# Performance work log

Measured on AMD Instinct MI355X. Metric: run time of the kernel, lower is better.

The kernel has to match this reference:

```python
import jax, jax.numpy as jnp
import numpy as np

D_MODEL = 1024
N_HEADS = 16
D_K = D_MODEL // N_HEADS


def setup_inputs() -> dict:
    key = jax.random.key(0)
    ks = jax.random.split(key, 12)
    B, S, D, H = 2, 2048, D_MODEL, N_HEADS
    s = 1.0 / np.sqrt(D)
    inp = {
        "x": jax.random.normal(ks[0], (B, S, D), jnp.float32),
        "Wq": jax.random.normal(ks[1], (D, D), jnp.float32) * s,
        "bq": jnp.zeros((D,), jnp.float32),
        "Wk": jax.random.normal(ks[2], (D, D), jnp.float32) * s,
        "bk": jnp.zeros((D,), jnp.float32),
        "Wv": jax.random.normal(ks[3], (D, D), jnp.float32) * s,
        "bv": jnp.zeros((D,), jnp.float32),
        "Wo": jax.random.normal(ks[4], (D, D), jnp.float32) * s,
        "bo": jnp.zeros((D,), jnp.float32),
        "Wp": jax.random.normal(ks[5], (D, H), jnp.float32) * s,
        "bp": jnp.zeros((H,), jnp.float32),
        "alpha": jax.random.normal(ks[6], (H,), jnp.float32) * 0.1,
    }
    return inp


def reference(x, Wq, bq, Wk, bk, Wv, bv, Wo, bo, Wp, bp, alpha):
    B, S, D = x.shape
    H, dk = N_HEADS, D_K
    scale = dk ** -0.5
    # projections -> (B, H, S, dk)
    Q = (x @ Wq + bq).reshape(B, S, H, dk).transpose(0, 2, 1, 3)
    K = (x @ Wk + bk).reshape(B, S, H, dk).transpose(0, 2, 1, 3)
    V = (x @ Wv + bv).reshape(B, S, H, dk).transpose(0, 2, 1, 3)
    scores = jnp.einsum("bhid,bhjd->bhij", Q, K) * scale  # (B,H,S,S)
    # phase derived from x: (B,S,H) -> (B,H,S)
    phase = (x @ Wp + bp).transpose(0, 2, 1)
    # coherence(i,j) = cos(phi_i - phi_j), per batch/head
    coherence = jnp.cos(phase[:, :, :, None] - phase[:, :, None, :])
    scores = scores + alpha[None, :, None, None] * coherence
    attn = jax.nn.softmax(scores, axis=-1)
    out = jnp.einsum("bhij,bhjd->bhid", attn, V)  # (B,H,S,dk)
    out = out.transpose(0, 2, 1, 3).reshape(B, S, D)
    return out @ Wo + bo
```

## Files before the change

kernel.cpp:

```cpp
#include <hip/hip_runtime.h>
#include <math.h>


#define S_LEN 2048
#define NHEADS 16

typedef __attribute__((ext_vector_type(8))) short short8;
typedef __attribute__((ext_vector_type(4))) float floatx4;
typedef __attribute__((ext_vector_type(2))) float float2v;
typedef __attribute__((ext_vector_type(4))) unsigned int uintx4;

__device__ inline unsigned short f2bf(float f) {
    union { float f; unsigned int i; } v; v.f = f;
    unsigned int u = v.i;
    return (unsigned short)((u + 0x7fffu + ((u >> 16) & 1u)) >> 16);
}
__device__ inline unsigned int pack2_bf16(float hi, float lo) {
    union { float f; unsigned int u; } a, b; a.f = hi; b.f = lo;
    return __builtin_amdgcn_perm(a.u, b.u, 0x07060302u);
}
__device__ inline void async_copy16(const unsigned short* src, unsigned short* dst_lds) {
    __builtin_amdgcn_global_load_lds(
        (const __attribute__((address_space(1))) unsigned int*)(src),
        (__attribute__((address_space(3))) unsigned int*)(dst_lds), 16, 0, 0);
}
__device__ inline void async_copy4(const float* src, float* dst_lds) {
    __builtin_amdgcn_global_load_lds(
        (const __attribute__((address_space(1))) unsigned int*)(src),
        (__attribute__((address_space(3))) unsigned int*)(dst_lds), 4, 0, 0);
}

__global__ __launch_bounds__(256) void prep_kernel(
    const float* __restrict__ x, const float* __restrict__ Wp,
    const float* __restrict__ bp,
    const float* __restrict__ w0, const float* __restrict__ w1,
    const float* __restrict__ w2, const float* __restrict__ w3,
    unsigned short* __restrict__ d0, unsigned short* __restrict__ d1,
    unsigned short* __restrict__ d2, unsigned short* __restrict__ d3,
    float* __restrict__ cosP, float* __restrict__ sinP,
    unsigned short* __restrict__ xb) {
    __shared__ __align__(16) unsigned short shmem[64 * 72];
    int t = threadIdx.x;
    if (blockIdx.x < 4096) {
        float* red = reinterpret_cast<float*>(shmem);
        int bid = blockIdx.x;
        int b = bid >> 11, s = bid & 2047;
        int h = t & 15, c = t >> 4;
        const float* xr = x + (size_t)bid * 1024;
        {
            float4 xv = *reinterpret_cast<const float4*>(&xr[t * 4]);
            uint2 o;
            o.x = (unsigned int)f2bf(xv.x) | ((unsigned int)f2bf(xv.y) << 16);
            o.y = (unsigned int)f2bf(xv.z) | ((unsigned int)f2bf(xv.w) << 16);
            *reinterpret_cast<uint2*>(&xb[(size_t)bid * 1024 + t * 4]) = o;
        }
        float acc = 0.f;
#pragma unroll 8
        for (int kk = 0; kk < 64; kk++) {
            int k = c * 64 + kk;
            acc += xr[k] * Wp[k * 16 + h];
        }
        red[t] = acc;
        __syncthreads();
        if (t < 16) {
            float sum = 0.f;
#pragma unroll
            for (int c2 = 0; c2 < 16; c2++) sum += red[c2 * 16 + t];
            sum += bp[t];
            float sv, cv;
            __sincosf(sum, &sv, &cv);
            size_t o = ((size_t)b * NHEADS + t) * S_LEN + s;
            cosP[o] = cv; sinP[o] = sv;
        }
    } else {
        unsigned short (*tile)[72] = reinterpret_cast<unsigned short (*)[72]>(shmem);
        int bid = blockIdx.x - 4096;
        int mat = bid >> 8;
        int tl  = bid & 255;
        int tr = tl >> 4, tc = tl & 15;
        const float* src    = (mat == 0) ? w0 : (mat == 1) ? w1 : (mat == 2) ? w2 : w3;
        unsigned short* dst = (mat == 0) ? d0 : (mat == 1) ? d1 : (mat == 2) ? d2 : d3;
        int col = t & 63, rbase = (t >> 6) * 16;
#pragma unroll
        for (int i = 0; i < 16; i++) {
            int row = rbase + i;
            tile[row][col] = f2bf(src[(size_t)(tr * 64 + row) * 1024 + tc * 64 + col]);
        }
        __syncthreads();
#pragma unroll
        for (int i = 0; i < 16; i++) {
            int row = rbase + i;
            dst[(size_t)(tc * 64 + row) * 1024 + tr * 64 + col] = tile[col][row];
        }
    }
}

template <int MT>
__global__ __launch_bounds__(256) void gemm_bt(
    const unsigned short* __restrict__ A, const unsigned short* __restrict__ BT,
    int N, int mode,
    const float* __restrict__ b0, const float* __restrict__ b1,
    const float* __restrict__ b2,
    unsigned short* __restrict__ o0, unsigned short* __restrict__ o1,
    unsigned short* __restrict__ o2, float* __restrict__ of) {
    __shared__ __align__(16) unsigned short As[MT * 32];
    __shared__ __align__(16) unsigned short Bs[128 * 32];
    const int K = 1024;
    const int MI = MT / 32;
    int t = threadIdx.x;
    int mBase = blockIdx.x * MT;
    int nBase = blockIdx.y * 128;
    int w = t >> 6, lane = t & 63, l15 = lane & 15, quad = lane >> 4;
    int wm = (w & 1) * (MT / 2), wn = (w >> 1) * 64;
    floatx4 acc[MI][4];
#pragma unroll
    for (int i = 0; i < MI; i++)
#pragma unroll
        for (int j = 0; j < 4; j++) acc[i][j] = (floatx4){0.f, 0.f, 0.f, 0.f};

    int arow = t >> 2, aseg = (t & 3) * 8;
    for (int k0 = 0; k0 < K; k0 += 32) {
        __syncthreads();
#pragma unroll
        for (int i = 0; i < MT / 64; i++)
            async_copy16(&A[(size_t)(mBase + i * 64 + arow) * K + k0 + aseg],
                         &As[(i * 64 + arow) * 32 + aseg]);
#pragma unroll
        for (int i = 0; i < 2; i++)
            async_copy16(&BT[(size_t)(nBase + i * 64 + arow) * K + k0 + aseg],
                         &Bs[(i * 64 + arow) * 32 + aseg]);
        __syncthreads();
        short8 af[MI], bfr[4];
#pragma unroll
        for (int mi = 0; mi < MI; mi++)
            af[mi] = *reinterpret_cast<const short8*>(&As[(wm + mi * 16 + l15) * 32 + quad * 8]);
#pragma unroll
        for (int ni = 0; ni < 4; ni++)
            bfr[ni] = *reinterpret_cast<const short8*>(&Bs[(wn + ni * 16 + l15) * 32 + quad * 8]);
#pragma unroll
        for (int mi = 0; mi < MI; mi++)
#pragma unroll
            for (int ni = 0; ni < 4; ni++)
                acc[mi][ni] = __builtin_amdgcn_mfma_f32_16x16x32_bf16(af[mi], bfr[ni], acc[mi][ni], 0, 0, 0);
    }

#pragma unroll
    for (int mi = 0; mi < MI; mi++) {
        int rowB = mBase + wm + mi * 16 + quad * 4;
#pragma unroll
        for (int ni = 0; ni < 4; ni++) {
            int col = nBase + wn + ni * 16 + l15;
            if (mode == 0) {
                float bias = b0[col];
#pragma unroll
                for (int r = 0; r < 4; r++) {
                    of[(size_t)(rowB + r) * N + col] = acc[mi][ni][r] + bias;
                }
            } else {
                int mat = col >> 10, nn = col & 1023;
                int h = nn >> 6, d = nn & 63;
                int b = rowB >> 11, sidx = rowB & 2047;
                if (mat == 2) {
                    float bv = b2[nn];
                    int jj = sidx & 63;
                    int a2 = jj >> 5, c2 = (jj >> 4) & 1, bb = jj & 15;
                    size_t rowOff = ((size_t)((b * NHEADS + h) * 64 + d)) * S_LEN +
                                    (sidx & ~63) + a2 * 32 + c2;
#pragma unroll
                    for (int r = 0; r < 4; r++)
                        o2[rowOff + 2 * (bb + r)] = f2bf(acc[mi][ni][r] + bv);
                } else {
                    const float* bias  = (mat == 0) ? b0 : b1;
                    unsigned short* op = (mat == 0) ? o0 : o1;
                    float bv = bias[nn];
                    float scl = (mat == 0) ? 0.18033688f : 1.0f;
#pragma unroll
                    for (int r = 0; r < 4; r++) {
                        float cv = (acc[mi][ni][r] + bv) * scl;
                        op[(((size_t)b * NHEADS + h) * S_LEN + (sidx + r)) * 64 + d] = f2bf(cv);
                    }
                }
            }
        }
    }
}

__global__ __launch_bounds__(256, 2) void attn_kernel(
    const unsigned short* __restrict__ Qg, const unsigned short* __restrict__ Kg,
    const unsigned short* __restrict__ VTg,
    const float* __restrict__ cosP, const float* __restrict__ sinP,
    const float* __restrict__ alpha, unsigned short* __restrict__ ctx) {
    __shared__ __align__(16) unsigned short KsB[2][64 * 64];
    __shared__ __align__(16) unsigned short VtB[2][64 * 64];
    __shared__ __align__(16) float csB[2][128];
    __shared__ __align__(16) unsigned short Plb[4][32 * 72];

    int x = blockIdx.x;
    int bh = (x & 7) * 4 + (x >> 7);
    int qt = (x >> 3) & 15;
    int t = threadIdx.x, w = t >> 6, lane = t & 63, l15 = lane & 15, quad = lane >> 4;
    int m0 = qt * 128 + w * 32;
    size_t base = (size_t)bh * (S_LEN * 64);
    size_t phBase = (size_t)bh * S_LEN;
    const float L2E = 1.44269504f;

    int sj0 = t >> 3, sg = t & 7;
    int srot = ((sg - (sj0 & 7)) & 7) * 8;
    int sj1 = sj0 + 32;

    short8 qf[2][2];
#pragma unroll
    for (int rh = 0; rh < 2; rh++)
#pragma unroll
        for (int c = 0; c < 2; c++)
            qf[rh][c] = *reinterpret_cast<const short8*>(
                &Qg[base + (size_t)(m0 + rh * 16 + l15) * 64 + c * 32 + quad * 8]);

    float alph = alpha[bh & 15] * L2E;
    float2v ci2[2][2], si2[2][2];
#pragma unroll
    for (int rh = 0; rh < 2; rh++)
#pragma unroll
        for (int hh = 0; hh < 2; hh++) {
            size_t o = phBase + m0 + rh * 16 + quad * 4 + hh * 2;
            ci2[rh][hh] = (float2v){alph * cosP[o], alph * cosP[o + 1]};
            si2[rh][hh] = (float2v){alph * sinP[o], alph * sinP[o + 1]};
        }

    {
        async_copy16(&Kg[base + (size_t)sj0 * 64 + srot], &KsB[0][t * 8]);
        async_copy16(&Kg[base + (size_t)sj1 * 64 + srot], &KsB[0][(t + 256) * 8]);
        async_copy16(&VTg[base + (size_t)sj0 * S_LEN + srot], &VtB[0][t * 8]);
        async_copy16(&VTg[base + (size_t)sj1 * S_LEN + srot], &VtB[0][(t + 256) * 8]);
        if (w == 2)      async_copy4(&cosP[phBase + lane], &csB[0][lane]);
        else if (w == 3) async_copy4(&sinP[phBase + lane], &csB[0][64 + lane]);
    }

    floatx4 oacc[2][4], lacc[2];
#pragma unroll
    for (int rh = 0; rh < 2; rh++) {
#pragma unroll
        for (int tt = 0; tt < 4; tt++) oacc[rh][tt] = (floatx4){0.f, 0.f, 0.f, 0.f};
        lacc[rh] = (floatx4){0.f, 0.f, 0.f, 0.f};
    }
    const short8 ones8 = {(short)0x3F80, (short)0x3F80, (short)0x3F80, (short)0x3F80,
                          (short)0x3F80, (short)0x3F80, (short)0x3F80, (short)0x3F80};

    int rot = l15 & 7;
    int cb0 = 16 * ((quad + rot) & 7);
    int cb1 = 16 * ((quad + 4 + rot) & 7);

    for (int kt = 0; kt < 32; kt++) {
        int p = kt & 1;
        __syncthreads();
        if (kt < 31) {
            int kn = kt + 1, pn = p ^ 1;
            async_copy16(&Kg[base + (size_t)(kn * 64 + sj0) * 64 + srot], &KsB[pn][t * 8]);
            async_copy16(&Kg[base + (size_t)(kn * 64 + sj1) * 64 + srot], &KsB[pn][(t + 256) * 8]);
            async_copy16(&VTg[base + (size_t)sj0 * S_LEN + kn * 64 + srot], &VtB[pn][t * 8]);
            async_copy16(&VTg[base + (size_t)sj1 * S_LEN + kn * 64 + srot], &VtB[pn][(t + 256) * 8]);
            if (w == 2)      async_copy4(&cosP[phBase + kn * 64 + lane], &csB[pn][lane]);
            else if (w == 3) async_copy4(&sinP[phBase + kn * 64 + lane], &csB[pn][64 + lane]);
        }

        floatx4 st[2][4];
#pragma unroll
        for (int jt = 0; jt < 4; jt++) {
            const char* kr = (const char*)&KsB[p][(jt * 16 + l15) * 64];
            short8 kf0 = *reinterpret_cast<const short8*>(kr + cb0);
            short8 kf1 = *reinterpret_cast<const short8*>(kr + cb1);
#pragma unroll
            for (int rh = 0; rh < 2; rh++) {
                floatx4 s = (floatx4){0.f, 0.f, 0.f, 0.f};
                s = __builtin_amdgcn_mfma_f32_16x16x32_bf16(qf[rh][0], kf0, s, 0, 0, 0);
                s = __builtin_amdgcn_mfma_f32_16x16x32_bf16(qf[rh][1], kf1, s, 0, 0, 0);
                st[rh][jt] = s;
            }
        }

        float cjv[4], sjv[4];
#pragma unroll
        for (int jt = 0; jt < 4; jt++) {
            cjv[jt] = csB[p][jt * 16 + l15];
            sjv[jt] = csB[p][64 + jt * 16 + l15];
        }

        unsigned int* pl = reinterpret_cast<unsigned int*>(&Plb[w][0]);
#pragma unroll
        for (int rh = 0; rh < 2; rh++)
#pragma unroll
            for (int rp = 0; rp < 2; rp++) {
                float2v a0, a1, a2, a3;
                {
                    float2v s0 = (float2v){st[rh][0][rp * 2], st[rh][0][rp * 2 + 1]};
                    float2v s1 = (float2v){st[rh][1][rp * 2], st[rh][1][rp * 2 + 1]};
                    float2v s2 = (float2v){st[rh][2][rp * 2], st[rh][2][rp * 2 + 1]};
                    float2v s3 = (float2v){st[rh][3][rp * 2], st[rh][3][rp * 2 + 1]};
                    a0 = si2[rh][rp] * sjv[0] + (ci2[rh][rp] * cjv[0] + s0);
                    a1 = si2[rh][rp] * sjv[1] + (ci2[rh][rp] * cjv[1] + s1);
                    a2 = si2[rh][rp] * sjv[2] + (ci2[rh][rp] * cjv[2] + s2);
                    a3 = si2[rh][rp] * sjv[3] + (ci2[rh][rp] * cjv[3] + s3);
                }
                int row = rh * 16 + quad * 4 + rp * 2;
                pl[row * 36 + l15]      = pack2_bf16(__builtin_amdgcn_exp2f(a1.x),
                                                     __builtin_amdgcn_exp2f(a0.x));
                pl[row * 36 + 16 + l15] = pack2_bf16(__builtin_amdgcn_exp2f(a3.x),
                                                     __builtin_amdgcn_exp2f(a2.x));
                pl[(row + 1) * 36 + l15]      = pack2_bf16(__builtin_amdgcn_exp2f(a1.y),
                                                           __builtin_amdgcn_exp2f(a0.y));
                pl[(row + 1) * 36 + 16 + l15] = pack2_bf16(__builtin_amdgcn_exp2f(a3.y),
                                                           __builtin_amdgcn_exp2f(a2.y));
            }

        short8 pf[2][2];
#pragma unroll
        for (int rh = 0; rh < 2; rh++)
#pragma unroll
            for (int c = 0; c < 2; c++)
                pf[rh][c] = *reinterpret_cast<const short8*>(
                    &Plb[w][(rh * 16 + l15) * 72 + c * 32 + quad * 8]);

#pragma unroll
        for (int c = 0; c < 2; c++) {
            int cb = c ? cb1 : cb0;
#pragma unroll
            for (int tt = 0; tt < 4; tt++) {
                const char* vr = (const char*)&VtB[p][(tt * 16 + l15) * 64];
                short8 vf = *reinterpret_cast<const short8*>(vr + cb);
                oacc[0][tt] = __builtin_amdgcn_mfma_f32_16x16x32_bf16(pf[0][c], vf, oacc[0][tt], 0, 0, 0);
                oacc[1][tt] = __builtin_amdgcn_mfma_f32_16x16x32_bf16(pf[1][c], vf, oacc[1][tt], 0, 0, 0);
            }
            lacc[0] = __builtin_amdgcn_mfma_f32_16x16x32_bf16(pf[0][c], ones8, lacc[0], 0, 0, 0);
            lacc[1] = __builtin_amdgcn_mfma_f32_16x16x32_bf16(pf[1][c], ones8, lacc[1], 0, 0, 0);
        }
    }

    int b = bh >> 4, h = bh & 15;
#pragma unroll
    for (int rh = 0; rh < 2; rh++) {
        float inv[4];
#pragma unroll
        for (int r = 0; r < 4; r++) inv[r] = 1.0f / lacc[rh][r];
#pragma unroll
        for (int tt = 0; tt < 4; tt++)
#pragma unroll
            for (int r = 0; r < 4; r++) {
                int srow = m0 + rh * 16 + quad * 4 + r;
                ctx[((size_t)(b * S_LEN + srow)) * 1024 + h * 64 + tt * 16 + l15] =
                    f2bf(oacc[rh][tt][r] * inv[r]);
            }
    }
}

extern "C" void kernel_launch(void* const* d_in, const int* in_sizes, int n_in,
                              void* d_out, int out_size, void* d_ws, size_t ws_size,
                              hipStream_t stream) {
    const float* x     = (const float*)d_in[0];
    const float* Wq    = (const float*)d_in[1];
    const float* bq    = (const float*)d_in[2];
    const float* Wk    = (const float*)d_in[3];
    const float* bk    = (const float*)d_in[4];
    const float* Wv    = (const float*)d_in[5];
    const float* bv    = (const float*)d_in[6];
    const float* Wo    = (const float*)d_in[7];
    const float* bo    = (const float*)d_in[8];
    const float* Wp    = (const float*)d_in[9];
    const float* bp    = (const float*)d_in[10];
    const float* alpha = (const float*)d_in[11];
    float* out = (float*)d_out;

    const size_t MB = 1048576;
    char* ws = (char*)d_ws;
    unsigned short* WT   = (unsigned short*)(ws);
    unsigned short* WoT  = (unsigned short*)(ws + 6 * MB);
    unsigned short* xb   = (unsigned short*)(ws + 8 * MB);
    unsigned short* ctx  = (unsigned short*)(ws + 8 * MB);
    unsigned short* Qw   = (unsigned short*)(ws + 16 * MB);
    unsigned short* Kw   = (unsigned short*)(ws + 24 * MB);
    unsigned short* VTg  = (unsigned short*)(ws + 32 * MB);
    float* cosP          = (float*)(ws + 40 * MB);
    float* sinP          = (float*)(ws + 40 * MB + 262144);

    prep_kernel<<<dim3(5120), dim3(256), 0, stream>>>(
        x, Wp, bp, Wq, Wk, Wv, Wo,
        WT, WT + 1048576, WT + 2097152, WoT, cosP, sinP, xb);
    gemm_bt<128><<<dim3(32, 24), dim3(256), 0, stream>>>(
        xb, WT, 3072, 1, bq, bk, bv, Qw, Kw, VTg, (float*)nullptr);
    attn_kernel<<<dim3(512), dim3(256), 0, stream>>>(
        Qw, Kw, VTg, cosP, sinP, alpha, ctx);
    gemm_bt<64><<<dim3(64, 8), dim3(256), 0, stream>>>(
        ctx, WoT, 1024, 0, bo, bo, bo,
        (unsigned short*)nullptr, (unsigned short*)nullptr,
        (unsigned short*)nullptr, out);
}
```

Baseline: 217.1 us.

## Software-pipeline PV matmul one tile behind QK and softmax with setprio hints

Defers the P·V MFMA for tile kt-1 into iteration kt so it interleaves with the QK^T MFMAs and exp computation of the current tile, using triple-buffered V tiles and double-buffered per-wave P buffers. Adds s_setprio around MFMA sections to favor matrix issue across waves. A drain step after the loop processes the final tile. This costs extra LDS and register pressure, which may affect occupancy at two blocks per CU.

```diff
diff --git a/kernel.cpp b/kernel.cpp
--- a/kernel.cpp
+++ b/kernel.cpp
@@ -191,9 +191,9 @@
     const float* __restrict__ cosP, const float* __restrict__ sinP,
     const float* __restrict__ alpha, unsigned short* __restrict__ ctx) {
     __shared__ __align__(16) unsigned short KsB[2][64 * 64];
-    __shared__ __align__(16) unsigned short VtB[2][64 * 64];
+    __shared__ __align__(16) unsigned short VtB[3][64 * 64];
     __shared__ __align__(16) float csB[2][128];
-    __shared__ __align__(16) unsigned short Plb[4][32 * 72];
+    __shared__ __align__(16) unsigned short Plb[2][4][32 * 72];
 
     int x = blockIdx.x;
     int bh = (x & 7) * 4 + (x >> 7);
@@ -254,16 +254,17 @@
         int p = kt & 1;
         __syncthreads();
         if (kt < 31) {
-            int kn = kt + 1, pn = p ^ 1;
+            int kn = kt + 1, pn = kn & 1, vn = kn % 3;
             async_copy16(&Kg[base + (size_t)(kn * 64 + sj0) * 64 + srot], &KsB[pn][t * 8]);
             async_copy16(&Kg[base + (size_t)(kn * 64 + sj1) * 64 + srot], &KsB[pn][(t + 256) * 8]);
-            async_copy16(&VTg[base + (size_t)sj0 * S_LEN + kn * 64 + srot], &VtB[pn][t * 8]);
-            async_copy16(&VTg[base + (size_t)sj1 * S_LEN + kn * 64 + srot], &VtB[pn][(t + 256) * 8]);
+            async_copy16(&VTg[base + (size_t)sj0 * S_LEN + kn * 64 + srot], &VtB[vn][t * 8]);
+            async_copy16(&VTg[base + (size_t)sj1 * S_LEN + kn * 64 + srot], &VtB[vn][(t + 256) * 8]);
             if (w == 2)      async_copy4(&cosP[phBase + kn * 64 + lane], &csB[pn][lane]);
             else if (w == 3) async_copy4(&sinP[phBase + kn * 64 + lane], &csB[pn][64 + lane]);
         }
 
         floatx4 st[2][4];
+        __builtin_amdgcn_s_setprio(1);
 #pragma unroll
         for (int jt = 0; jt < 4; jt++) {
             const char* kr = (const char*)&KsB[p][(jt * 16 + l15) * 64];
@@ -277,6 +278,34 @@
                 st[rh][jt] = s;
             }
         }
+        __builtin_amdgcn_s_setprio(0);
+
+        if (kt > 0) {
+            int vp = (kt - 1) % 3;
+            const unsigned short* plprev = &Plb[(kt - 1) & 1][w][0];
+            short8 pf[2][2];
+#pragma unroll
+            for (int rh = 0; rh < 2; rh++)
+#pragma unroll
+                for (int c = 0; c < 2; c++)
+                    pf[rh][c] = *reinterpret_cast<const short8*>(
+                        &plprev[(rh * 16 + l15) * 72 + c * 32 + quad * 8]);
+            __builtin_amdgcn_s_setprio(1);
+#pragma unroll
+            for (int c = 0; c < 2; c++) {
+                int cb = c ? cb1 : cb0;
+#pragma unroll
+                for (int tt = 0; tt < 4; tt++) {
+                    const char* vr = (const char*)&VtB[vp][(tt * 16 + l15) * 64];
+                    short8 vf = *reinterpret_cast<const short8*>(vr + cb);
+                    oacc[0][tt] = __builtin_amdgcn_mfma_f32_16x16x32_bf16(pf[0][c], vf, oacc[0][tt], 0, 0, 0);
+                    oacc[1][tt] = __builtin_amdgcn_mfma_f32_16x16x32_bf16(pf[1][c], vf, oacc[1][tt], 0, 0, 0);
+                }
+                lacc[0] = __builtin_amdgcn_mfma_f32_16x16x32_bf16(pf[0][c], ones8, lacc[0], 0, 0, 0);
+                lacc[1] = __builtin_amdgcn_mfma_f32_16x16x32_bf16(pf[1][c], ones8, lacc[1], 0, 0, 0);
+            }
+            __builtin_amdgcn_s_setprio(0);
+        }
 
         float cjv[4], sjv[4];
 #pragma unroll
@@ -284,8 +313,7 @@
             cjv[jt] = csB[p][jt * 16 + l15];
             sjv[jt] = csB[p][64 + jt * 16 + l15];
         }
-
-        unsigned int* pl = reinterpret_cast<unsigned int*>(&Plb[w][0]);
+        unsigned int* pl = reinterpret_cast<unsigned int*>(&Plb[p][w][0]);
 #pragma unroll
         for (int rh = 0; rh < 2; rh++)
 #pragma unroll
@@ -311,21 +339,24 @@
                 pl[(row + 1) * 36 + 16 + l15] = pack2_bf16(__builtin_amdgcn_exp2f(a3.y),
                                                            __builtin_amdgcn_exp2f(a2.y));
             }
-
+    }
+
+    {
+        const unsigned short* plprev = &Plb[1][w][0];
+        int vp = 1;
         short8 pf[2][2];
 #pragma unroll
         for (int rh = 0; rh < 2; rh++)
 #pragma unroll
             for (int c = 0; c < 2; c++)
                 pf[rh][c] = *reinterpret_cast<const short8*>(
-                    &Plb[w][(rh * 16 + l15) * 72 + c * 32 + quad * 8]);
-
+                    &plprev[(rh * 16 + l15) * 72 + c * 32 + quad * 8]);
 #pragma unroll
         for (int c = 0; c < 2; c++) {
             int cb = c ? cb1 : cb0;
 #pragma unroll
             for (int tt = 0; tt < 4; tt++) {
-                const char* vr = (const char*)&VtB[p][(tt * 16 + l15) * 64];
+                const char* vr = (const char*)&VtB[vp][(tt * 16 + l15) * 64];
                 short8 vf = *reinterpret_cast<const short8*>(vr + cb);
                 oacc[0][tt] = __builtin_amdgcn_mfma_f32_16x16x32_bf16(pf[0][c], vf, oacc[0][tt], 0, 0, 0);
                 oacc[1][tt] = __builtin_amdgcn_mfma_f32_16x16x32_bf16(pf[1][c], vf, oacc[1][tt], 0, 0, 0);
```

After: 219.5 us. Within noise of the previous version (+1.1%).

## Double GEMM K-step to 64 with rotated LDS swizzle to avoid bank conflicts

Applied to the files above, without the earlier changes.

The projection GEMM now stages 64-wide K slices per iteration instead of 32, which halves the number of barrier pairs and load rounds. The shared-memory tiles use a per-row rotation of the 16-byte chunks so that MFMA fragment reads avoid bank conflicts. The cost is twice the LDS footprint per block, which could lower occupancy. Within each slice, the two MFMAs per accumulator pair up chunks that share the same k-offset on both the A and B sides.

```diff
diff --git a/kernel.cpp b/kernel.cpp
--- a/kernel.cpp
+++ b/kernel.cpp
@@ -103,8 +103,8 @@
     const float* __restrict__ b2,
     unsigned short* __restrict__ o0, unsigned short* __restrict__ o1,
     unsigned short* __restrict__ o2, float* __restrict__ of) {
-    __shared__ __align__(16) unsigned short As[MT * 32];
-    __shared__ __align__(16) unsigned short Bs[128 * 32];
+    __shared__ __align__(16) unsigned short As[MT * 64];
+    __shared__ __align__(16) unsigned short Bs[128 * 64];
     const int K = 1024;
     const int MI = MT / 32;
     int t = threadIdx.x;
@@ -118,30 +118,45 @@
 #pragma unroll
         for (int j = 0; j < 4; j++) acc[i][j] = (floatx4){0.f, 0.f, 0.f, 0.f};
 
-    int arow = t >> 2, aseg = (t & 3) * 8;
-    for (int k0 = 0; k0 < K; k0 += 32) {
+    int rot = l15 & 7;
+    int cb0 = 16 * ((quad + rot) & 7);
+    int cb1 = 16 * ((quad + 4 + rot) & 7);
+
+    for (int k0 = 0; k0 < K; k0 += 64) {
         __syncthreads();
 #pragma unroll
-        for (int i = 0; i < MT / 64; i++)
-            async_copy16(&A[(size_t)(mBase + i * 64 + arow) * K + k0 + aseg],
-                         &As[(i * 64 + arow) * 32 + aseg]);
-#pragma unroll
-        for (int i = 0; i < 2; i++)
-            async_copy16(&BT[(size_t)(nBase + i * 64 + arow) * K + k0 + aseg],
-                         &Bs[(i * 64 + arow) * 32 + aseg]);
+        for (int i = 0; i < MT / 32; i++) {
+            int ci = i * 256 + t;
+            int row = ci >> 3, scc = ((ci & 7) - (row & 7)) & 7;
+            async_copy16(&A[(size_t)(mBase + row) * K + k0 + scc * 8], &As[ci * 8]);
+        }
+#pragma unroll
+        for (int i = 0; i < 4; i++) {
+            int ci = i * 256 + t;
+            int row = ci >> 3, scc = ((ci & 7) - (row & 7)) & 7;
+            async_copy16(&BT[(size_t)(nBase + row) * K + k0 + scc * 8], &Bs[ci * 8]);
+        }
         __syncthreads();
-        short8 af[MI], bfr[4];
+        short8 af[MI][2], bfr[4][2];
+#pragma unroll
+        for (int mi = 0; mi < MI; mi++) {
+            const char* ar = (const char*)&As[(wm + mi * 16 + l15) * 64];
+            af[mi][0] = *reinterpret_cast<const short8*>(ar + cb0);
+            af[mi][1] = *reinterpret_cast<const short8*>(ar + cb1);
+        }
+#pragma unroll
+        for (int ni = 0; ni < 4; ni++) {
+            const char* br = (const char*)&Bs[(wn + ni * 16 + l15) * 64];
+            bfr[ni][0] = *reinterpret_cast<const short8*>(br + cb0);
+            bfr[ni][1] = *reinterpret_cast<const short8*>(br + cb1);
+        }
 #pragma unroll
         for (int mi = 0; mi < MI; mi++)
-            af[mi] = *reinterpret_cast<const short8*>(&As[(wm + mi * 16 + l15) * 32 + quad * 8]);
-#pragma unroll
-        for (int ni = 0; ni < 4; ni++)
-            bfr[ni] = *reinterpret_cast<const short8*>(&Bs[(wn + ni * 16 + l15) * 32 + quad * 8]);
-#pragma unroll
-        for (int mi = 0; mi < MI; mi++)
-#pragma unroll
-            for (int ni = 0; ni < 4; ni++)
-                acc[mi][ni] = __builtin_amdgcn_mfma_f32_16x16x32_bf16(af[mi], bfr[ni], acc[mi][ni], 0, 0, 0);
+#pragma unroll
+            for (int ni = 0; ni < 4; ni++) {
+                acc[mi][ni] = __builtin_amdgcn_mfma_f32_16x16x32_bf16(af[mi][0], bfr[ni][0], acc[mi][ni], 0, 0, 0);
+                acc[mi][ni] = __builtin_amdgcn_mfma_f32_16x16x32_bf16(af[mi][1], bfr[ni][1], acc[mi][ni], 0, 0, 0);
+            }
     }
 
 #pragma unroll
```

Measured after the change: 232.0 us. 6.9% more time.
